# Performance work log

Hardware: AMD Instinct MI355X
Metric: run time of the kernel (lower is better)

Reference implementation:

```python
import jax, jax.numpy as jnp
import numpy as np

N = 8192        # nodes
E = 131072      # edges (avg degree 16)
D_EMB = 128     # node embedding dim -> MLP input = 3*D_EMB = 384
F_IN = 64       # raw node feature dim
N_CLS = 7       # downstream model classes


def setup_inputs() -> dict:
    key = jax.random.key(0)
    ks = jax.random.split(key, 8)
    x = jax.random.normal(ks[0], (N, F_IN), dtype=jnp.float32)
    embed = jax.random.normal(ks[1], (N, D_EMB), dtype=jnp.float32)
    row = jax.random.randint(ks[2], (E,), 0, N, dtype=jnp.int64) if jax.config.read('jax_enable_x64') else jax.random.randint(ks[2], (E,), 0, N).astype(jnp.int32)
    col = jax.random.randint(ks[3], (E,), 0, N).astype(row.dtype)
    adj_data = jnp.ones((E,), dtype=jnp.float32)
    W1 = jax.random.normal(ks[4], (3 * D_EMB, 64), dtype=jnp.float32) * (1.0 / np.sqrt(3 * D_EMB))
    b1 = jnp.zeros((64,), dtype=jnp.float32)
    W2 = jax.random.normal(ks[5], (64, 1), dtype=jnp.float32) * 0.125
    b2 = jnp.zeros((1,), dtype=jnp.float32)
    Wg = jax.random.normal(ks[6], (F_IN, N_CLS), dtype=jnp.float32) * 0.125
    return {"x": x, "embed": embed, "row": row, "col": col, "adj_data": adj_data,
            "W1": W1, "b1": b1, "W2": W2, "b2": b2, "Wg": Wg, "nodeid": 0}


def reference(x, embed, row, col, adj_data, W1, b1, W2, b2, Wg, nodeid):
    n = embed.shape[0]
    # edge gather: copy_src / copy_dst + broadcast target-node embedding  -> [E, 3*D]
    f1 = embed[row]
    f2 = embed[col]
    fs = jnp.broadcast_to(embed[nodeid][None, :], f1.shape)
    feats = jnp.concatenate([f1, f2, fs], axis=-1)
    # tiny 2-layer MLP -> per-edge logit
    h = jax.nn.relu(feats @ W1 + b1)
    log_alpha = (h @ W2 + b2).reshape(-1)             # [E]
    # concrete_sample with training=False: plain sigmoid gate
    gate = jax.nn.sigmoid(log_alpha)
    # sparse mask -> dense (duplicate indices sum, as torch.sparse coalesce does)
    mask = jnp.zeros((n, n), dtype=x.dtype).at[row, col].add(gate)
    sym_mask = 0.5 * (mask + mask.T)
    adj_dense = jnp.zeros((n, n), dtype=x.dtype).at[row, col].add(adj_data)
    masked_adj = adj_dense * sym_mask
    diag = jnp.arange(n)
    masked_adj = masked_adj.at[diag, diag].set(0.0)   # * (1 - eye)
    # downstream model: one dense-adjacency GCN layer
    logits = masked_adj @ (x @ Wg)                    # [N, N_CLS]
    node_pred = logits[nodeid]
    return jax.nn.softmax(node_pred, axis=0)
```

## Files before the change

### kernel.cpp

```cpp
#include <hip/hip_runtime.h>
#include <math.h>

#define DEMB 128
#define HID 64
#define NCLS 7
#define FIN 64

#define PROD 128
#define SEG_SLOTS 64
#define FLATCAP 128
#define TAG 0x5EED0000
#define TAGMASK 0xFFFF0000

struct __align__(16) Ent { int r; int c; float adj; float gate; float y[NCLS]; float pad; };

__global__ void __launch_bounds__(256) k_all(
    const float* __restrict__ x, const float* __restrict__ embed,
    const int* __restrict__ row, const int* __restrict__ col,
    const float* __restrict__ adj_data,
    const float* __restrict__ W1, const float* __restrict__ b1,
    const float* __restrict__ W2, const float* __restrict__ b2,
    const float* __restrict__ Wg, const int* __restrict__ nodeid,
    Ent* __restrict__ gout, int* gcount, float* __restrict__ out, int E) {
  const int t = threadIdx.x;
  const int b = blockIdx.x;

  if (b < PROD) {
    __shared__ int lcnt;
    __shared__ int lfr[SEG_SLOTS], lfc[SEG_SLOTS];
    __shared__ float lfa[SEG_SLOTS];
    __shared__ float feats[3 * DEMB];
    __shared__ float hp[16][HID];
    __shared__ float swg[FIN * NCLS];
    __shared__ float sb1[HID], sw2[HID];
    __shared__ __align__(16) float sW1[3 * DEMB * HID];

    if (t == 0) lcnt = 0;
    for (int i = t; i < FIN * NCLS; i += 256) swg[i] = Wg[i];
    if (t < HID) { sb1[t] = b1[t]; sw2[t] = W2[t]; }
    __syncthreads();

    const int nid = *nodeid;

    const int per = (E + PROD - 1) / PROD;
    const int e0 = b * per;
    const int e1 = (e0 + per < E) ? (e0 + per) : E;

    if (((e0 & 3) == 0) && (((e1 - e0) & 3) == 0)) {
      const int4* row4 = reinterpret_cast<const int4*>(row + e0);
      const int4* col4 = reinterpret_cast<const int4*>(col + e0);
      const int ngrp = (e1 - e0) >> 2;
      for (int g = t; g < ngrp; g += 256) {
        const int4 r4 = row4[g];
        const int4 c4 = col4[g];
        const int eb = e0 + g * 4;
        #pragma unroll
        for (int q = 0; q < 4; ++q) {
          const int rr = (&r4.x)[q];
          const int cc = (&c4.x)[q];
          if (rr == nid || cc == nid) {
            int i = atomicAdd(&lcnt, 1);
            if (i < SEG_SLOTS) { lfr[i] = rr; lfc[i] = cc; lfa[i] = adj_data[eb + q]; }
          }
        }
      }
    } else {
      for (int e = e0 + t; e < e1; e += 256) {
        const int rr = row[e];
        const int cc = col[e];
        if (rr == nid || cc == nid) {
          int i = atomicAdd(&lcnt, 1);
          if (i < SEG_SLOTS) { lfr[i] = rr; lfc[i] = cc; lfa[i] = adj_data[e]; }
        }
      }
    }
    if (t < DEMB) feats[2 * DEMB + t] = embed[(size_t)nid * DEMB + t];
    __syncthreads();

    int cnt = lcnt;
    if (cnt > SEG_SLOTS) cnt = SEG_SLOTS;

    if (cnt > 0) {
      const float b2v = *b2;
      const int ug = t & 15;
      const int ks = t >> 4;
      float4* sW1v = reinterpret_cast<float4*>(sW1);
      const float4* W1v = reinterpret_cast<const float4*>(W1);
      for (int g = t; g < (3 * DEMB * HID) / 4; g += 256) sW1v[g] = W1v[g];

      for (int i = 0; i < cnt; ++i) {
        const int r = lfr[i];
        const int c = lfc[i];
        if (t < DEMB) feats[t] = embed[(size_t)r * DEMB + t];
        else          feats[DEMB + (t - DEMB)] = embed[(size_t)c * DEMB + (t - DEMB)];
        float xv = 0.0f;
        if (t < FIN && r == nid) xv = x[(size_t)c * FIN + t];
        __syncthreads();

        float4 acc = make_float4(0.f, 0.f, 0.f, 0.f);
        const int k0 = ks * 24;
        #pragma unroll
        for (int kk = 0; kk < 24; ++kk) {
          const int k = k0 + kk;
          const float4 w = sW1v[(size_t)k * 16 + ug];
          const float f = feats[k];
          acc.x = fmaf(f, w.x, acc.x);
          acc.y = fmaf(f, w.y, acc.y);
          acc.z = fmaf(f, w.z, acc.z);
          acc.w = fmaf(f, w.w, acc.w);
        }
        reinterpret_cast<float4*>(hp)[ks * 16 + ug] = acc;
        __syncthreads();

        if (t < HID) {
          float h = sb1[t];
          #pragma unroll
          for (int s = 0; s < 16; ++s) h += hp[s][t];
          h = fmaxf(h, 0.0f);
          float part = h * sw2[t];
          #pragma unroll
          for (int off = 32; off > 0; off >>= 1)
            part += __shfl_down(part, off, 64);

          float yv[NCLS];
          #pragma unroll
          for (int cc = 0; cc < NCLS; ++cc) {
            float pr = xv * swg[t * NCLS + cc];
            #pragma unroll
            for (int off = 32; off > 0; off >>= 1)
              pr += __shfl_down(pr, off, 64);
            yv[cc] = pr;
          }
          if (t == 0) {
            const float gate = 1.0f / (1.0f + expf(-(part + b2v)));
            Ent en;
            en.r = r; en.c = c; en.adj = lfa[i]; en.gate = gate;
            #pragma unroll
            for (int cc = 0; cc < NCLS; ++cc) en.y[cc] = yv[cc];
            en.pad = 0.0f;
            gout[(size_t)b * SEG_SLOTS + i] = en;
          }
        }
        __syncthreads();
      }
    }
    if (t == 0)
      __hip_atomic_store(&gcount[b], TAG | cnt, __ATOMIC_RELEASE,
                         __HIP_MEMORY_SCOPE_AGENT);
    return;
  }

  __shared__ int cnts[PROD];
  __shared__ int offs[PROD + 1];
  __shared__ Ent flat[FLATCAP];

  if (t < PROD) {
    int v;
    for (;;) {
      v = __hip_atomic_load(&gcount[t], __ATOMIC_ACQUIRE, __HIP_MEMORY_SCOPE_AGENT);
      if ((v & TAGMASK) == TAG) break;
      __builtin_amdgcn_s_sleep(1);
    }
    cnts[t] = v & 0xFFFF;
  }
  __syncthreads();
  if (t == 0) {
    int acc = 0;
    for (int s = 0; s < PROD; ++s) { offs[s] = acc; acc += cnts[s]; }
    offs[PROD] = acc;
  }
  __syncthreads();

  int nE = offs[PROD];
  if (nE > FLATCAP) nE = FLATCAP;

  if (t < PROD) {
    const int o = offs[t];
    const int cb = cnts[t];
    for (int i = 0; i < cb; ++i)
      if (o + i < FLATCAP) flat[o + i] = gout[(size_t)t * SEG_SLOTS + i];
  }
  __syncthreads();

  if (t < 64) {
    const int nid = *nodeid;
    float myc[NCLS];
    #pragma unroll
    for (int cc = 0; cc < NCLS; ++cc) myc[cc] = 0.0f;

    for (int p = t; p < nE; p += 64) {
      const Ent ep = flat[p];
      if (ep.r != nid || ep.c == nid) continue;
      const int j = ep.c;
      bool first = true;
      float A = 0.0f, G1 = 0.0f, G2 = 0.0f;
      for (int q = 0; q < nE; ++q) {
        const int qr = flat[q].r, qc = flat[q].c;
        if (qr == nid && qc == j) {
          if (q < p) first = false;
          A += flat[q].adj;
          G1 += flat[q].gate;
        }
        if (qc == nid && qr == j) G2 += flat[q].gate;
      }
      if (!first) continue;
      const float s = A * 0.5f * (G1 + G2);
      #pragma unroll
      for (int cc = 0; cc < NCLS; ++cc) myc[cc] = fmaf(s, ep.y[cc], myc[cc]);
    }

    #pragma unroll
    for (int cc = 0; cc < NCLS; ++cc) {
      #pragma unroll
      for (int off = 32; off > 0; off >>= 1)
        myc[cc] += __shfl_down(myc[cc], off, 64);
    }
    if (t == 0) {
      float m = myc[0];
      #pragma unroll
      for (int cc = 1; cc < NCLS; ++cc) m = fmaxf(m, myc[cc]);
      float sum = 0.0f, ex[NCLS];
      #pragma unroll
      for (int cc = 0; cc < NCLS; ++cc) { ex[cc] = expf(myc[cc] - m); sum += ex[cc]; }
      #pragma unroll
      for (int cc = 0; cc < NCLS; ++cc) out[cc] = ex[cc] / sum;
    }
  }
}

extern "C" void kernel_launch(void* const* d_in, const int* in_sizes, int n_in,
                              void* d_out, int out_size, void* d_ws, size_t ws_size,
                              hipStream_t stream) {
  const float* x      = (const float*)d_in[0];
  const float* embed  = (const float*)d_in[1];
  const int*   row    = (const int*)d_in[2];
  const int*   col    = (const int*)d_in[3];
  const float* adj    = (const float*)d_in[4];
  const float* W1     = (const float*)d_in[5];
  const float* b1     = (const float*)d_in[6];
  const float* W2     = (const float*)d_in[7];
  const float* b2     = (const float*)d_in[8];
  const float* Wg     = (const float*)d_in[9];
  const int*   nodeid = (const int*)d_in[10];
  float* out = (float*)d_out;
  const int E = in_sizes[2];

  char* ws = (char*)d_ws;
  Ent* gout = (Ent*)ws;
  int* gcnt = (int*)(ws + (size_t)PROD * SEG_SLOTS * sizeof(Ent));

  hipLaunchKernelGGL(k_all, dim3(PROD + 1), dim3(256), 0, stream,
                     x, embed, row, col, adj, W1, b1, W2, b2, Wg, nodeid,
                     gout, gcnt, out, E);
}
```

Measured before the change: 13.81 us.

## Batch embedding gathers for up to eight edges and parallelize consumer prefix scan

Producer blocks now load the embedding rows and x rows for up to eight selected edges into registers in one pass and then stage them in shared memory. The per-edge MLP loop then runs from shared memory, so the global-load latency for each edge is no longer serialized with its compute. The consumer block replaces a serial 128-element prefix sum on one thread with a wave-level shuffle scan. It adds shared-memory usage and a __syncthreads inside divergent branches, which is legal only because every thread reaches a matching barrier.

```diff
diff --git a/kernel.cpp b/kernel.cpp
--- a/kernel.cpp
+++ b/kernel.cpp
@@ -9,6 +9,7 @@
 #define PROD 128
 #define SEG_SLOTS 64
 #define FLATCAP 128
+#define MAXB 8
 #define TAG 0x5EED0000
 #define TAGMASK 0xFFFF0000
 
@@ -29,7 +30,8 @@
     __shared__ int lcnt;
     __shared__ int lfr[SEG_SLOTS], lfc[SEG_SLOTS];
     __shared__ float lfa[SEG_SLOTS];
-    __shared__ float feats[3 * DEMB];
+    __shared__ float feats_all[MAXB][3 * DEMB];
+    __shared__ float sx[MAXB][FIN];
     __shared__ float hp[16][HID];
     __shared__ float swg[FIN * NCLS];
     __shared__ float sb1[HID], sw2[HID];
@@ -74,7 +76,6 @@
         }
       }
     }
-    if (t < DEMB) feats[2 * DEMB + t] = embed[(size_t)nid * DEMB + t];
     __syncthreads();
 
     int cnt = lcnt;
@@ -88,60 +89,88 @@
       const float4* W1v = reinterpret_cast<const float4*>(W1);
       for (int g = t; g < (3 * DEMB * HID) / 4; g += 256) sW1v[g] = W1v[g];
 
-      for (int i = 0; i < cnt; ++i) {
-        const int r = lfr[i];
-        const int c = lfc[i];
-        if (t < DEMB) feats[t] = embed[(size_t)r * DEMB + t];
-        else          feats[DEMB + (t - DEMB)] = embed[(size_t)c * DEMB + (t - DEMB)];
-        float xv = 0.0f;
-        if (t < FIN && r == nid) xv = x[(size_t)c * FIN + t];
+      for (int base = 0; base < cnt; base += MAXB) {
+        const int nb = (cnt - base < MAXB) ? (cnt - base) : MAXB;
+
+        float fr[MAXB], fn[MAXB], xv[MAXB];
+        #pragma unroll
+        for (int i = 0; i < MAXB; ++i) {
+          fr[i] = 0.f; fn[i] = 0.f; xv[i] = 0.f;
+          if (i < nb) {
+            const int r = lfr[base + i];
+            const int c = lfc[base + i];
+            if (t < DEMB) {
+              fr[i] = embed[(size_t)r * DEMB + t];
+              fn[i] = embed[(size_t)nid * DEMB + t];
+            } else {
+              fr[i] = embed[(size_t)c * DEMB + (t - DEMB)];
+            }
+            if (t < FIN && r == nid) xv[i] = x[(size_t)c * FIN + t];
+          }
+        }
+        #pragma unroll
+        for (int i = 0; i < MAXB; ++i) {
+          if (i < nb) {
+            if (t < DEMB) {
+              feats_all[i][t] = fr[i];
+              feats_all[i][2 * DEMB + t] = fn[i];
+            } else {
+              feats_all[i][DEMB + (t - DEMB)] = fr[i];
+            }
+            if (t < FIN) sx[i][t] = xv[i];
+          }
+        }
         __syncthreads();
 
-        float4 acc = make_float4(0.f, 0.f, 0.f, 0.f);
-        const int k0 = ks * 24;
-        #pragma unroll
-        for (int kk = 0; kk < 24; ++kk) {
-          const int k = k0 + kk;
-          const float4 w = sW1v[(size_t)k * 16 + ug];
-          const float f = feats[k];
-          acc.x = fmaf(f, w.x, acc.x);
-          acc.y = fmaf(f, w.y, acc.y);
-          acc.z = fmaf(f, w.z, acc.z);
-          acc.w = fmaf(f, w.w, acc.w);
-        }
-        reinterpret_cast<float4*>(hp)[ks * 16 + ug] = acc;
-        __syncthreads();
-
-        if (t < HID) {
-          float h = sb1[t];
+        for (int i = 0; i < nb; ++i) {
+          float4 acc = make_float4(0.f, 0.f, 0.f, 0.f);
+          const int k0 = ks * 24;
           #pragma unroll
-          for (int s = 0; s < 16; ++s) h += hp[s][t];
-          h = fmaxf(h, 0.0f);
-          float part = h * sw2[t];
-          #pragma unroll
-          for (int off = 32; off > 0; off >>= 1)
-            part += __shfl_down(part, off, 64);
-
-          float yv[NCLS];
-          #pragma unroll
-          for (int cc = 0; cc < NCLS; ++cc) {
-            float pr = xv * swg[t * NCLS + cc];
+          for (int kk = 0; kk < 24; ++kk) {
+            const int k = k0 + kk;
+            const float4 w = sW1v[(size_t)k * 16 + ug];
+            const float f = feats_all[i][k];
+            acc.x = fmaf(f, w.x, acc.x);
+            acc.y = fmaf(f, w.y, acc.y);
+            acc.z = fmaf(f, w.z, acc.z);
+            acc.w = fmaf(f, w.w, acc.w);
+          }
+          reinterpret_cast<float4*>(hp)[ks * 16 + ug] = acc;
+          __syncthreads();
+
+          if (t < HID) {
+            float h = sb1[t];
+            #pragma unroll
+            for (int s = 0; s < 16; ++s) h += hp[s][t];
+            h = fmaxf(h, 0.0f);
+            float part = h * sw2[t];
             #pragma unroll
             for (int off = 32; off > 0; off >>= 1)
-              pr += __shfl_down(pr, off, 64);
-            yv[cc] = pr;
-          }
-          if (t == 0) {
-            const float gate = 1.0f / (1.0f + expf(-(part + b2v)));
-            Ent en;
-            en.r = r; en.c = c; en.adj = lfa[i]; en.gate = gate;
+              part += __shfl_down(part, off, 64);
+
+            const float xl = sx[i][t & 63];
+            float yv[NCLS];
             #pragma unroll
-            for (int cc = 0; cc < NCLS; ++cc) en.y[cc] = yv[cc];
-            en.pad = 0.0f;
-            gout[(size_t)b * SEG_SLOTS + i] = en;
-          }
-        }
-        __syncthreads();
+            for (int cc = 0; cc < NCLS; ++cc) {
+              float pr = xl * swg[(t & 63) * NCLS + cc];
+              #pragma unroll
+              for (int off = 32; off > 0; off >>= 1)
+                pr += __shfl_down(pr, off, 64);
+              yv[cc] = pr;
+            }
+            if (t == 0) {
+              const float gate = 1.0f / (1.0f + expf(-(part + b2v)));
+              Ent en;
+              en.r = lfr[base + i]; en.c = lfc[base + i];
+              en.adj = lfa[base + i]; en.gate = gate;
+              #pragma unroll
+              for (int cc = 0; cc < NCLS; ++cc) en.y[cc] = yv[cc];
+              en.pad = 0.0f;
+              gout[(size_t)b * SEG_SLOTS + base + i] = en;
+            }
+          }
+          __syncthreads();
+        }
       }
     }
     if (t == 0)
@@ -152,6 +181,7 @@
 
   __shared__ int cnts[PROD];
   __shared__ int offs[PROD + 1];
+  __shared__ int wtot[2];
   __shared__ Ent flat[FLATCAP];
 
   if (t < PROD) {
@@ -163,11 +193,23 @@
     }
     cnts[t] = v & 0xFFFF;
   }
-  __syncthreads();
-  if (t == 0) {
-    int acc = 0;
-    for (int s = 0; s < PROD; ++s) { offs[s] = acc; acc += cnts[s]; }
-    offs[PROD] = acc;
+  if (t < PROD) {
+    const int lane = t & 63;
+    const int w = t >> 6;
+    const int v = cnts[t];
+    int sc = v;
+    #pragma unroll
+    for (int off = 1; off < 64; off <<= 1) {
+      const int nbr = __shfl_up(sc, off, 64);
+      if (lane >= off) sc += nbr;
+    }
+    if (lane == 63) wtot[w] = sc;
+    __syncthreads();
+    const int wbase = (w == 1) ? wtot[0] : 0;
+    offs[t] = wbase + sc - v;
+    if (t == PROD - 1) offs[PROD] = wbase + sc;
+  } else {
+    __syncthreads();
   }
   __syncthreads();
 
```

New measurement: 13.54 us. 1.02x faster.
